# Performance work log

Measured on AMD Instinct MI355X. Metric: run time of the kernel, lower is better.

## Reference

```python
import jax, jax.numpy as jnp
import numpy as np

B, H, SQ, SK, DH = 1, 32, 2048, 2048, 128


def setup_inputs() -> dict:
    key = jax.random.key(0)
    k1, k2, k3 = jax.random.split(key, 3)
    logits = jax.random.normal(k1, (B, H, SQ, SK), dtype=jnp.float32)
    value = jax.random.normal(k2, (B, H, SK, DH), dtype=jnp.float32)
    # learnable per-head sink scalars (init zeros in the module; use small randn
    # here so the sink path is actually exercised)
    sinks = jax.random.normal(k3, (H,), dtype=jnp.float32) * 0.1
    return {"logits": logits, "value": value, "sinks": sinks}


def reference(logits, value, sinks):
    # sink column broadcast to [B, H, Sq, 1]; sinks viewed with H at dim -3
    sink_col = jnp.broadcast_to(
        sinks.reshape(1, H, 1, 1), logits.shape[:-1] + (1,)
    ).astype(logits.dtype)
    combined = jnp.concatenate([logits, sink_col], axis=-1)  # [B,H,Sq,Sk+1]
    m = jax.lax.stop_gradient(jnp.max(combined, axis=-1, keepdims=True))
    probs = jax.nn.softmax(combined - m, axis=-1)[..., :-1]  # drop sink col
    probs = probs.astype(value.dtype)
    return jnp.matmul(probs, value)  # [B,H,Sq,Dh]
```

## Files before the change

kernel.cpp:

```cpp
#include <hip/hip_runtime.h>


#define H  32
#define SQ 2048
#define SK 2048
#define DH 128

typedef __attribute__((ext_vector_type(8))) short short8;
typedef __attribute__((ext_vector_type(4))) float f32x4;

__device__ __forceinline__ short f2bf(float f) {
  union { float f; unsigned u; } v; v.f = f;
  unsigned r = v.u + 0x7fffu + ((v.u >> 16) & 1u);
  return (short)(r >> 16);
}

__global__ __launch_bounds__(256) void convert_v_kernel(const float* __restrict__ v,
                                                        short* __restrict__ vswz) {
  int tid  = blockIdx.x * 256 + threadIdx.x;
  int lane = tid & 63;
  int rest = tid >> 6;
  int nt   = rest & 7;
  int hkb  = rest >> 3;
  int kb   = hkb & 63;
  int h    = hkb >> 6;
  int col  = nt * 16 + (lane & 15);
  int krow = kb * 32 + (lane >> 4) * 8;
  const float* src = v + ((size_t)(h * SK + krow)) * DH + col;
  short8 p;
#pragma unroll
  for (int j = 0; j < 8; ++j) p[j] = f2bf(src[(size_t)j * DH]);
  *(short8*)(vswz + (size_t)tid * 8) = p;
}

__global__ __launch_bounds__(256) void attn_sink_kernel(const float* __restrict__ logits,
                                                        const short* __restrict__ vswz,
                                                        const float* __restrict__ sinks,
                                                        float* __restrict__ out) {
  const int wg   = blockIdx.x;
  const int h    = wg >> 5;
  const int qt   = wg & 31;
  const int wave = threadIdx.x >> 6;
  const int lane = threadIdx.x & 63;
  const int row16 = lane & 15;
  const int quad  = lane >> 4;

  const int qrow = qt * 64 + wave * 16 + row16;
  const float* lptr = logits + ((size_t)(h * SQ + qrow)) * SK + quad * 8;
  const short* vbase = vswz + ((size_t)h * 64 * 8 * 512) + lane * 8;

  f32x4 acc[8];
#pragma unroll
  for (int i = 0; i < 8; ++i) acc[i] = (f32x4){0.f, 0.f, 0.f, 0.f};
  float dsum = 0.f;

  for (int kb = 0; kb < 64; ++kb) {
    float4 a0 = *(const float4*)(lptr);
    float4 a1 = *(const float4*)(lptr + 4);
    lptr += 32;
    float e0 = __expf(a0.x), e1 = __expf(a0.y), e2 = __expf(a0.z), e3 = __expf(a0.w);
    float e4 = __expf(a1.x), e5 = __expf(a1.y), e6 = __expf(a1.z), e7 = __expf(a1.w);
    dsum += ((e0 + e1) + (e2 + e3)) + ((e4 + e5) + (e6 + e7));
    short8 afrag;
    afrag[0] = f2bf(e0); afrag[1] = f2bf(e1); afrag[2] = f2bf(e2); afrag[3] = f2bf(e3);
    afrag[4] = f2bf(e4); afrag[5] = f2bf(e5); afrag[6] = f2bf(e6); afrag[7] = f2bf(e7);
    const short* vblk = vbase + (size_t)kb * 8 * 512;
#pragma unroll
    for (int nt = 0; nt < 8; ++nt) {
      short8 bfrag = *(const short8*)(vblk + nt * 512);
      acc[nt] = __builtin_amdgcn_mfma_f32_16x16x32_bf16(afrag, bfrag, acc[nt], 0, 0, 0);
    }
  }

  dsum += __shfl_xor(dsum, 16);
  dsum += __shfl_xor(dsum, 32);
  float denom = dsum + __expf(sinks[h]);

  float* obase = out + ((size_t)(h * SQ + qt * 64 + wave * 16)) * DH;
#pragma unroll
  for (int r = 0; r < 4; ++r) {
    float inv = 1.0f / __shfl(denom, quad * 4 + r);
#pragma unroll
    for (int nt = 0; nt < 8; ++nt) {
      obase[(size_t)(quad * 4 + r) * DH + nt * 16 + row16] = acc[nt][r] * inv;
    }
  }
}

extern "C" void kernel_launch(void* const* d_in, const int* in_sizes, int n_in,
                              void* d_out, int out_size, void* d_ws, size_t ws_size,
                              hipStream_t stream) {
  const float* logits = (const float*)d_in[0];
  const float* value  = (const float*)d_in[1];
  const float* sinks  = (const float*)d_in[2];
  float* out  = (float*)d_out;
  short* vswz = (short*)d_ws;

  convert_v_kernel<<<4096, 256, 0, stream>>>(value, vswz);
  attn_sink_kernel<<<1024, 256, 0, stream>>>(logits, vswz, sinks, out);
}
```

Measured before the change: 784.0 us.

## Prefetch logits nontemporally, compute row sums via MFMA, and reorder head-major grid

```diff
diff --git a/kernel.cpp b/kernel.cpp
--- a/kernel.cpp
+++ b/kernel.cpp
@@ -9,80 +9,91 @@
 typedef __attribute__((ext_vector_type(8))) short short8;
 typedef __attribute__((ext_vector_type(4))) float f32x4;
 
-__device__ __forceinline__ short f2bf(float f) {
+__device__ __forceinline__ short f2bf_ru(float f) {
   union { float f; unsigned u; } v; v.f = f;
-  unsigned r = v.u + 0x7fffu + ((v.u >> 16) & 1u);
-  return (short)(r >> 16);
+  return (short)((v.u + 0x8000u) >> 16);
 }
 
 __global__ __launch_bounds__(256) void convert_v_kernel(const float* __restrict__ v,
                                                         short* __restrict__ vswz) {
-  int tid  = blockIdx.x * 256 + threadIdx.x;
-  int lane = tid & 63;
-  int rest = tid >> 6;
-  int nt   = rest & 7;
-  int hkb  = rest >> 3;
-  int kb   = hkb & 63;
-  int h    = hkb >> 6;
-  int col  = nt * 16 + (lane & 15);
-  int krow = kb * 32 + (lane >> 4) * 8;
-  const float* src = v + ((size_t)(h * SK + krow)) * DH + col;
-  short8 p;
-#pragma unroll
-  for (int j = 0; j < 8; ++j) p[j] = f2bf(src[(size_t)j * DH]);
-  *(short8*)(vswz + (size_t)tid * 8) = p;
+  int tid = blockIdx.x * 256 + threadIdx.x;
+  int c4  = tid & 31;
+  int k   = (tid >> 5) & (SK - 1);
+  int h   = tid >> 16;
+  f32x4 val = *(const f32x4*)(v + ((size_t)(h * SK + k)) * DH + c4 * 4);
+  int kb   = k >> 5;
+  int krem = k & 31;
+  int qd   = krem >> 3;
+  int j    = krem & 7;
+  int colbase = c4 * 4;
+  int nt = colbase >> 4;
+  short* dst = vswz + ((((size_t)(h * 64 + kb)) * 8 + nt) * 512) + j;
+  int lanebase = qd * 16 + (colbase & 15);
+  dst[(size_t)(lanebase + 0) * 8] = f2bf_ru(val.x);
+  dst[(size_t)(lanebase + 1) * 8] = f2bf_ru(val.y);
+  dst[(size_t)(lanebase + 2) * 8] = f2bf_ru(val.z);
+  dst[(size_t)(lanebase + 3) * 8] = f2bf_ru(val.w);
 }
 
-__global__ __launch_bounds__(256) void attn_sink_kernel(const float* __restrict__ logits,
-                                                        const short* __restrict__ vswz,
-                                                        const float* __restrict__ sinks,
-                                                        float* __restrict__ out) {
-  const int wg   = blockIdx.x;
-  const int h    = wg >> 5;
-  const int qt   = wg & 31;
+__global__ __launch_bounds__(256, 4) void attn_sink_kernel(const float* __restrict__ logits,
+                                                           const short* __restrict__ vswz,
+                                                           const float* __restrict__ sinks,
+                                                           float* __restrict__ out) {
+  const int wg = blockIdx.x;
+  const int h  = wg & 31;
+  const int qt = wg >> 5;
   const int wave = threadIdx.x >> 6;
   const int lane = threadIdx.x & 63;
   const int row16 = lane & 15;
   const int quad  = lane >> 4;
 
   const int qrow = qt * 64 + wave * 16 + row16;
-  const float* lptr = logits + ((size_t)(h * SQ + qrow)) * SK + quad * 8;
-  const short* vbase = vswz + ((size_t)h * 64 * 8 * 512) + lane * 8;
+  const float* lp = logits + ((size_t)(h * SQ + qrow)) * SK + quad * 8;
+  const short* vbase = vswz + ((size_t)h * (64 * 8 * 512)) + lane * 8;
+
+  short8 ones;
+#pragma unroll
+  for (int i = 0; i < 8; ++i) ones[i] = (short)0x3F80;
 
   f32x4 acc[8];
 #pragma unroll
   for (int i = 0; i < 8; ++i) acc[i] = (f32x4){0.f, 0.f, 0.f, 0.f};
-  float dsum = 0.f;
+  f32x4 accd = (f32x4){0.f, 0.f, 0.f, 0.f};
+
+  f32x4 a0 = __builtin_nontemporal_load((const f32x4*)lp);
+  f32x4 a1 = __builtin_nontemporal_load((const f32x4*)lp + 1);
 
   for (int kb = 0; kb < 64; ++kb) {
-    float4 a0 = *(const float4*)(lptr);
-    float4 a1 = *(const float4*)(lptr + 4);
-    lptr += 32;
+    const f32x4* np = (const f32x4*)(lp + ((kb < 63) ? 32 : 0));
+    f32x4 na0 = __builtin_nontemporal_load(np);
+    f32x4 na1 = __builtin_nontemporal_load(np + 1);
+    lp += 32;
+
     float e0 = __expf(a0.x), e1 = __expf(a0.y), e2 = __expf(a0.z), e3 = __expf(a0.w);
     float e4 = __expf(a1.x), e5 = __expf(a1.y), e6 = __expf(a1.z), e7 = __expf(a1.w);
-    dsum += ((e0 + e1) + (e2 + e3)) + ((e4 + e5) + (e6 + e7));
-    short8 afrag;
-    afrag[0] = f2bf(e0); afrag[1] = f2bf(e1); afrag[2] = f2bf(e2); afrag[3] = f2bf(e3);
-    afrag[4] = f2bf(e4); afrag[5] = f2bf(e5); afrag[6] = f2bf(e6); afrag[7] = f2bf(e7);
-    const short* vblk = vbase + (size_t)kb * 8 * 512;
+    short8 af;
+    af[0] = f2bf_ru(e0); af[1] = f2bf_ru(e1); af[2] = f2bf_ru(e2); af[3] = f2bf_ru(e3);
+    af[4] = f2bf_ru(e4); af[5] = f2bf_ru(e5); af[6] = f2bf_ru(e6); af[7] = f2bf_ru(e7);
+
+    const short* vblk = vbase + (size_t)kb * (8 * 512);
+    accd = __builtin_amdgcn_mfma_f32_16x16x32_bf16(af, ones, accd, 0, 0, 0);
 #pragma unroll
     for (int nt = 0; nt < 8; ++nt) {
       short8 bfrag = *(const short8*)(vblk + nt * 512);
-      acc[nt] = __builtin_amdgcn_mfma_f32_16x16x32_bf16(afrag, bfrag, acc[nt], 0, 0, 0);
+      acc[nt] = __builtin_amdgcn_mfma_f32_16x16x32_bf16(af, bfrag, acc[nt], 0, 0, 0);
     }
+    a0 = na0; a1 = na1;
   }
 
-  dsum += __shfl_xor(dsum, 16);
-  dsum += __shfl_xor(dsum, 32);
-  float denom = dsum + __expf(sinks[h]);
-
+  const float es = __expf(sinks[h]);
   float* obase = out + ((size_t)(h * SQ + qt * 64 + wave * 16)) * DH;
 #pragma unroll
   for (int r = 0; r < 4; ++r) {
-    float inv = 1.0f / __shfl(denom, quad * 4 + r);
+    float inv = 1.0f / (accd[r] + es);
 #pragma unroll
     for (int nt = 0; nt < 8; ++nt) {
-      obase[(size_t)(quad * 4 + r) * DH + nt * 16 + row16] = acc[nt][r] * inv;
+      __builtin_nontemporal_store(acc[nt][r] * inv,
+                                  obase + (size_t)(quad * 4 + r) * DH + nt * 16 + row16);
     }
   }
 }
@@ -96,6 +107,6 @@
   float* out  = (float*)d_out;
   short* vswz = (short*)d_ws;
 
-  convert_v_kernel<<<4096, 256, 0, stream>>>(value, vswz);
+  convert_v_kernel<<<8192, 256, 0, stream>>>(value, vswz);
   attn_sink_kernel<<<1024, 256, 0, stream>>>(logits, vswz, sinks, out);
 }
```

After: 802.2 us. +2.3%, slower.
